# Kernel tuning notes

Measured on AMD Instinct MI355X. Metric: run time of the kernel, lower is better.

The kernel has to match this reference:

```python
import jax, jax.numpy as jnp
import numpy as np

B, S, HID, NH = 2, 2048, 2048, 16
HD = HID // NH  # 128
BASE = 10000.0


def rope_tables(seq_len, head_dim):
    inv_freq = 1.0 / (BASE ** (jnp.arange(0, head_dim, 2, dtype=jnp.float32) / head_dim))
    t = jnp.arange(seq_len, dtype=jnp.float32)
    freqs = jnp.einsum('i,j->ij', t, inv_freq)        # [s, d/2]
    emb = jnp.concatenate([freqs, freqs], axis=-1)     # [s, d]
    return jnp.cos(emb), jnp.sin(emb)


def apply_rotary(x, cos, sin):
    # x: [b, s, h, d]; cos/sin: [s, d]
    x1, x2 = x[..., ::2], x[..., 1::2]
    c = cos[None, :, None, ::2]
    s = sin[None, :, None, ::2]
    x1r = x1 * c - x2 * s
    x2r = x1 * s + x2 * c
    return jnp.stack([x1r, x2r], axis=-1).reshape(x.shape)


def setup_inputs() -> dict:
    key = jax.random.key(0)
    ks = jax.random.split(key, 5)
    scale = 1.0 / np.sqrt(HID)
    hidden_states = jax.random.normal(ks[0], (B, S, HID), jnp.float32)
    Wq = jax.random.normal(ks[1], (HID, HID), jnp.float32) * scale
    Wk = jax.random.normal(ks[2], (HID, HID), jnp.float32) * scale
    Wv = jax.random.normal(ks[3], (HID, HID), jnp.float32) * scale
    Wo = jax.random.normal(ks[4], (HID, HID), jnp.float32) * scale
    causal = jnp.tril(jnp.ones((S, S), dtype=bool))
    attention_mask = jnp.where(causal, 0.0, -1e9).astype(jnp.float32)[None, :, :]  # [1, S, S]
    return {'hidden_states': hidden_states, 'Wq': Wq, 'Wk': Wk, 'Wv': Wv,
            'Wo': Wo, 'attention_mask': attention_mask}


def reference(hidden_states, Wq, Wk, Wv, Wo, attention_mask):
    b, s, hid = hidden_states.shape
    q = (hidden_states @ Wq.T).reshape(b, s, NH, HD)
    k = (hidden_states @ Wk.T).reshape(b, s, NH, HD)
    v = (hidden_states @ Wv.T).reshape(b, s, NH, HD)
    cos, sin = rope_tables(s, HD)
    q = apply_rotary(q, cos, sin)
    k = apply_rotary(k, cos, sin)
    # [b, h, s, d]
    q = q.transpose(0, 2, 1, 3)
    k = k.transpose(0, 2, 1, 3)
    v = v.transpose(0, 2, 1, 3)
    scores = jnp.einsum('bhqd,bhkd->bhqk', q, k) / np.sqrt(HD).astype(np.float32)
    scores = scores + attention_mask[:, None, :, :]  # broadcast mask over heads
    probs = jax.nn.softmax(scores.astype(jnp.float32), axis=-1).astype(q.dtype)
    attn = jnp.einsum('bhqk,bhkd->bhqd', probs, v)
    attn = attn.transpose(0, 2, 1, 3).reshape(b, s, hid)
    return attn @ Wo.T
```

## Files before the change

kernel.cpp:

```cpp
#include <hip/hip_runtime.h>
#include <math.h>

typedef __attribute__((ext_vector_type(8))) short short8;
typedef __attribute__((ext_vector_type(4))) float f32x4;
typedef __attribute__((ext_vector_type(16))) float f32x16;
typedef __attribute__((ext_vector_type(4))) float fvec4;
typedef __attribute__((ext_vector_type(4))) unsigned short us4;
typedef __attribute__((ext_vector_type(2))) unsigned int uint2v;

#define DI __device__ __forceinline__
#define BARX asm volatile("s_barrier" ::: "memory")
#define WAITV6 asm volatile("s_waitcnt vmcnt(6)" ::: "memory")
#define WAITV0 asm volatile("s_waitcnt vmcnt(0)" ::: "memory")
#define WAITL0 asm volatile("s_waitcnt lgkmcnt(0)" ::: "memory")
#define SCHED0 __builtin_amdgcn_sched_barrier(0)

constexpr int BB = 2, SS = 2048, HIDc = 2048, NHc = 16, HDc = 128;
constexpr int MT = BB * SS;
constexpr int KC = HIDc;

constexpr size_t OFF_HB  = 0;
constexpr size_t OFF_WB  = OFF_HB + (size_t)MT * KC * 2;
constexpr size_t OFF_Q   = OFF_WB + (size_t)4 * HIDc * KC * 2;
constexpr size_t OFF_K   = OFF_Q  + (size_t)BB * NHc * SS * HDc * 2;
constexpr size_t OFF_V   = OFF_K  + (size_t)BB * NHc * SS * HDc * 2;
constexpr size_t OFF_ATT = OFF_V  + (size_t)BB * NHc * SS * HDc * 2;
constexpr size_t OFF_COS = OFF_ATT + (size_t)MT * HIDc * 2;
constexpr size_t OFF_SIN = OFF_COS + (size_t)SS * 32 * 4;
constexpr size_t WS_NEED = OFF_SIN + (size_t)SS * 32 * 4;

DI float bf2f(unsigned short u) { union { unsigned u; float f; } v; v.u = (unsigned)u << 16; return v.f; }
DI unsigned short f2bf(float f) {
  union { float f; unsigned u; } v; v.f = f;
  unsigned r = v.u + 0x7fffu + ((v.u >> 16) & 1u);
  return (unsigned short)(r >> 16);
}

DI void gload_lds16(const void* g, void* l) {
  __builtin_amdgcn_global_load_lds((const __attribute__((address_space(1))) void*)g,
                                   (__attribute__((address_space(3))) void*)l, 16, 0, 0);
}

DI unsigned cvtpk_bf16(float lo, float hi_) {
  unsigned r;
  asm("v_cvt_pk_bf16_f32 %0, %1, %2" : "=v"(r) : "v"(lo), "v"(hi_));
  return r;
}

__global__ void __launch_bounds__(256) cvt_kernel(
    const float* __restrict__ H,  const float* __restrict__ W0,
    const float* __restrict__ W1, const float* __restrict__ W2,
    const float* __restrict__ W3, unsigned short* __restrict__ dst,
    float* __restrict__ cosT, float* __restrict__ sinT)
{
  constexpr size_t HN = (size_t)MT * KC;
  constexpr size_t WN = (size_t)HIDc * KC;
  if (blockIdx.x >= 12288) {
    int idx = (blockIdx.x - 12288) * 256 + threadIdx.x;
    int t = idx >> 5, fi = idx & 31;
    float inv = powf(10000.0f, -(float)fi * (1.0f / 32.0f));
    float ang = (float)t * inv;
    cosT[idx] = cosf(ang);
    sinT[idx] = sinf(ang);
    return;
  }
  size_t e0 = ((size_t)blockIdx.x * 256 + threadIdx.x) * 8;
  const float* src; size_t off;
  if (e0 < HN) { src = H; off = e0; }
  else {
    size_t t = e0 - HN; int a = (int)(t >> 22);
    src = (a == 0) ? W0 : (a == 1) ? W1 : (a == 2) ? W2 : W3;
    off = t & (WN - 1);
  }
  fvec4 v0 = *(const fvec4*)(src + off);
  fvec4 v1 = *(const fvec4*)(src + off + 4);
  short8 o;
  o[0] = (short)f2bf(v0[0]); o[1] = (short)f2bf(v0[1]);
  o[2] = (short)f2bf(v0[2]); o[3] = (short)f2bf(v0[3]);
  o[4] = (short)f2bf(v1[0]); o[5] = (short)f2bf(v1[1]);
  o[6] = (short)f2bf(v1[2]); o[7] = (short)f2bf(v1[3]);
  *(short8*)(dst + e0) = o;
}

template<int NBX>
__global__ void __launch_bounds__(512, 2) gemm8p(
    const unsigned short* __restrict__ A,
    const unsigned short* __restrict__ Bw,
    void* __restrict__ dq, void* __restrict__ dk, void* __restrict__ dv,
    const float* __restrict__ cosT, const float* __restrict__ sinT)
{
  __shared__ __align__(16) unsigned short SL[8][128 * 64];
  const int tid = threadIdx.x, lane = tid & 63, w = tid >> 6;
  const int wm = w >> 2, wn = w & 3;
  const int ln15 = lane & 15, lq = lane >> 4;

  const int xcd = blockIdx.x & 7, idx = blockIdx.x >> 3;
  const int by = xcd * 2 + idx / NBX, bx = idx % NBX;
  const int m0 = by * 256, n0 = bx * 256;

  const int srow = tid >> 3;
  const int sc = (tid & 7) ^ (srow & 7);
  const unsigned short* Ab = A  + ((size_t)m0 + srow) * KC + sc * 8;
  const unsigned short* Bb = Bw + ((size_t)n0 + srow) * KC + sc * 8;

  constexpr int NT = KC / 64;
  auto stage = [&](int kt, bool isA, int half, int buf) {
    if (kt >= NT) return;
    const unsigned short* s = (isA ? Ab : Bb) + (size_t)(half * 128) * KC + kt * 64;
    int slot = (isA ? 0 : 4) + buf * 2 + half;
    unsigned short* d = &SL[slot][(size_t)(w * 64) * 8];
    gload_lds16(s, d);
    gload_lds16(s + (size_t)64 * KC, d + (size_t)512 * 8);
  };

  auto readA = [&](int buf, int q, int i, int ks) -> short8 {
    int rl = ((q & 1) << 6) + (i << 5) + (wm << 4) + ln15;
    return *(const short8*)&SL[buf * 2 + (q >> 1)]
        [rl * 64 + ((((ks << 2) + lq) ^ (rl & 7)) << 3)];
  };
  auto readB = [&](int buf, int j, int ks) -> short8 {
    int rl = ((wn & 1) << 6) + (j << 4) + ln15;
    return *(const short8*)&SL[4 + buf * 2 + (wn >> 1)]
        [rl * 64 + ((((ks << 2) + lq) ^ (rl & 7)) << 3)];
  };

  stage(0, true, 0, 0); stage(0, true, 1, 0);
  stage(0, false, 0, 0); stage(0, false, 1, 0);
  stage(1, false, 0, 1); stage(1, false, 1, 1); stage(1, true, 0, 1);
  WAITV6; BARX;

  f32x4 acc[8][4] = {};
  short8 bfr[4][2];
  constexpr int NIT = NT / 2;
  for (int t = 0; t < NIT; ++t) {
    const int k2 = 2 * t + 2, k3 = 2 * t + 3;
#pragma unroll
    for (int b = 0; b < 2; ++b) {
#pragma unroll
      for (int q = 0; q < 4; ++q) {
        short8 af[2][2];
#pragma unroll
        for (int i = 0; i < 2; ++i)
#pragma unroll
          for (int ks = 0; ks < 2; ++ks) af[i][ks] = readA(b, q, i, ks);
        if (q == 0) {
#pragma unroll
          for (int j = 0; j < 4; ++j)
#pragma unroll
            for (int ks = 0; ks < 2; ++ks) bfr[j][ks] = readB(b, j, ks);
        }
        if (b == 0) {
          if (q == 0) stage(2 * t + 1, true, 1, 1);
          else if (q == 1) stage(k2, false, 0, 0);
          else if (q == 2) stage(k2, false, 1, 0);
          else stage(k2, true, 0, 0);
        } else {
          if (q == 0) stage(k2, true, 1, 0);
          else if (q == 1) stage(k3, false, 0, 1);
          else if (q == 2) stage(k3, false, 1, 1);
          else stage(k3, true, 0, 1);
        }
        BARX;
        WAITL0; SCHED0;
        __builtin_amdgcn_s_setprio(1);
#pragma unroll
        for (int i = 0; i < 2; ++i)
#pragma unroll
          for (int j = 0; j < 4; ++j)
#pragma unroll
            for (int ks = 0; ks < 2; ++ks)
              acc[2 * q + i][j] = __builtin_amdgcn_mfma_f32_16x16x32_bf16(
                  af[i][ks], bfr[j][ks], acc[2 * q + i][j], 0, 0, 0);
        __builtin_amdgcn_s_setprio(0);
        if (q == 3) { if (t == NIT - 1) { WAITV0; } else { WAITV6; } }
        BARX;
      }
    }
  }

#pragma unroll
  for (int f = 0; f < 8; ++f)
#pragma unroll
    for (int j = 0; j < 4; ++j) {
      int col = n0 + wn * 64 + j * 16 + ln15;
      int z = col >> 11;
      int c2 = col & 2047;
      int h = c2 >> 7, d = c2 & 127;
      int m = m0 + 32 * f + 16 * wm + lq * 4;
      int b = m >> 11, s = m & 2047;
      if (z == 2) {
        us4 pk;
#pragma unroll
        for (int r = 0; r < 4; ++r) pk[r] = f2bf(acc[f][j][r]);
        *(us4*)((unsigned short*)dv + (((size_t)b * NHc + h) * HDc + d) * SS + s) = pk;
      } else {
        unsigned short* D = (unsigned short*)(z ? dk : dq);
        const int fi = (d >> 1) & 31;
        const bool odd = (d & 1) != 0;
#pragma unroll
        for (int r = 0; r < 4; ++r) {
          float v = acc[f][j][r];
          float p = __shfl_xor(v, 1);
          float cs = cosT[(size_t)(s + r) * 32 + fi];
          float sn = sinT[(size_t)(s + r) * 32 + fi];
          float y = odd ? (p * sn + v * cs) : (v * cs - p * sn);
          D[(((size_t)b * NHc + h) * SS + s + r) * HDc + d] = f2bf(y);
        }
      }
    }
}

template<int EPI, int NBX>
__global__ void __launch_bounds__(512, 2) gemm8(
    const unsigned short* __restrict__ A,
    const unsigned short* __restrict__ Bw,
    void* __restrict__ dq, void* __restrict__ dk, void* __restrict__ dv,
    const float* __restrict__ cosT, const float* __restrict__ sinT)
{
  __shared__ __align__(16) unsigned short Al[3][256 * 64];
  __shared__ __align__(16) unsigned short Bl[3][128 * 64];
  const int tid = threadIdx.x, lane = tid & 63, w = tid >> 6;
  const int wm = w >> 1, wn = w & 1;
  const int ln15 = lane & 15, lq = lane >> 4;

  const int xcd = blockIdx.x & 7, idx = blockIdx.x >> 3;
  const int by = xcd * 2 + idx / NBX, bx = idx % NBX;
  const int m0 = by * 256, n0 = bx * 128;

  const int srow = tid >> 3;
  const int sc = (tid & 7) ^ (srow & 7);
  const unsigned short* asrc[4];
  const unsigned short* bsrc[2];
#pragma unroll
  for (int l = 0; l < 4; ++l) asrc[l] = A  + (size_t)(m0 + l * 64 + srow) * KC + sc * 8;
#pragma unroll
  for (int l = 0; l < 2; ++l) bsrc[l] = Bw + (size_t)(n0 + l * 64 + srow) * KC + sc * 8;

  const int x7 = ln15 & 7;
  const int slA0 = (lq ^ x7) * 8;
  const int slA1 = ((4 + lq) ^ x7) * 8;
  int rA[4], rB[4];
#pragma unroll
  for (int i = 0; i < 4; ++i) rA[i] = (wm * 64 + i * 16 + ln15) * 64;
#pragma unroll
  for (int j = 0; j < 4; ++j) rB[j] = (wn * 64 + j * 16 + ln15) * 64;

  constexpr int NT = KC / 64;
  auto stA = [&](int kt, int buf, int l) {
    gload_lds16(asrc[l] + (size_t)kt * 64, &Al[buf][(size_t)(l * 512 + w * 64) * 8]);
  };
  auto stB = [&](int kt, int buf, int l) {
    gload_lds16(bsrc[l] + (size_t)kt * 64, &Bl[buf][(size_t)(l * 512 + w * 64) * 8]);
  };

  stA(0, 0, 0); stA(0, 0, 1); stA(0, 0, 2); stA(0, 0, 3); stB(0, 0, 0); stB(0, 0, 1);
  stA(1, 1, 0); stA(1, 1, 1); stA(1, 1, 2); stA(1, 1, 3); stB(1, 1, 0); stB(1, 1, 1);
  WAITV6; BARX;

  f32x4 acc[4][4] = {};
  int cb = 0, nb = 2;
  for (int kt = 0; kt < NT; ++kt) {
    const unsigned short* Ac = &Al[cb][0];
    const unsigned short* Bc = &Bl[cb][0];
    const bool pf = (kt + 2 < NT);
    short8 a01[2][2], a23[2][2], bf[4][2];

#pragma unroll
    for (int i = 0; i < 2; ++i) {
      a01[i][0] = *(const short8*)&Ac[rA[i] + slA0];
      a01[i][1] = *(const short8*)&Ac[rA[i] + slA1];
    }
#pragma unroll
    for (int j = 0; j < 4; ++j) {
      bf[j][0] = *(const short8*)&Bc[rB[j] + slA0];
      bf[j][1] = *(const short8*)&Bc[rB[j] + slA1];
    }
    if (pf) { stA(kt + 2, nb, 0); stA(kt + 2, nb, 1); stA(kt + 2, nb, 2); }
    BARX;
    WAITL0; SCHED0;
    __builtin_amdgcn_s_setprio(1);
#pragma unroll
    for (int i = 0; i < 2; ++i)
#pragma unroll
      for (int j = 0; j < 4; ++j)
#pragma unroll
        for (int k = 0; k < 2; ++k)
          acc[i][j] = __builtin_amdgcn_mfma_f32_16x16x32_bf16(a01[i][k], bf[j][k], acc[i][j], 0, 0, 0);
    __builtin_amdgcn_s_setprio(0);
    BARX;

#pragma unroll
    for (int i = 0; i < 2; ++i) {
      a23[i][0] = *(const short8*)&Ac[rA[2 + i] + slA0];
      a23[i][1] = *(const short8*)&Ac[rA[2 + i] + slA1];
    }
    if (pf) { stA(kt + 2, nb, 3); stB(kt + 2, nb, 0); stB(kt + 2, nb, 1); }
    BARX;
    WAITL0; SCHED0;
    __builtin_amdgcn_s_setprio(1);
#pragma unroll
    for (int i = 0; i < 2; ++i)
#pragma unroll
      for (int j = 0; j < 4; ++j)
#pragma unroll
        for (int k = 0; k < 2; ++k)
          acc[2 + i][j] = __builtin_amdgcn_mfma_f32_16x16x32_bf16(a23[i][k], bf[j][k], acc[2 + i][j], 0, 0, 0);
    __builtin_amdgcn_s_setprio(0);
    if (kt < NT - 2) { WAITV6; }
    else if (kt == NT - 2) { WAITV0; }
    BARX;

    cb = (cb == 2) ? 0 : cb + 1;
    nb = (nb == 2) ? 0 : nb + 1;
  }

  if (EPI == 1) {
    float* O = (float*)dq;
#pragma unroll
    for (int i = 0; i < 4; ++i)
#pragma unroll
      for (int j = 0; j < 4; ++j) {
        int col = n0 + wn * 64 + j * 16 + ln15;
        int m = m0 + wm * 64 + i * 16 + lq * 4;
#pragma unroll
        for (int r = 0; r < 4; ++r)
          O[(size_t)(m + r) * HIDc + col] = acc[i][j][r];
      }
  } else {
    unsigned short* V = (unsigned short*)dq;
#pragma unroll
    for (int i = 0; i < 4; ++i)
#pragma unroll
      for (int j = 0; j < 4; ++j) {
        int col = n0 + wn * 64 + j * 16 + ln15;
        int h = col >> 7, d = col & 127;
        int m = m0 + wm * 64 + i * 16 + lq * 4;
        int b = m >> 11, s = m & 2047;
        us4 pk;
#pragma unroll
        for (int r = 0; r < 4; ++r) pk[r] = f2bf(acc[i][j][r]);
        *(us4*)(V + (((size_t)b * NHc + h) * HDc + d) * SS + s) = pk;
      }
  }
}

__global__ void __launch_bounds__(512, 2) attn_kernel(
    const unsigned short* __restrict__ Qg,
    const unsigned short* __restrict__ Kg,
    const unsigned short* __restrict__ Vg,
    unsigned short* __restrict__ Og)
{
  __shared__ __align__(16) unsigned short Klds[2][128 * 128];
  __shared__ __align__(16) unsigned short Vlds[2][128 * 128];
  __shared__ __align__(16) unsigned short Plds[8][32 * 32];
  const int tid = threadIdx.x, lane = tid & 63, w = tid >> 6;
  const int l31 = lane & 31, hi = lane >> 5;

  const int wg = blockIdx.x;
  const int xcd = wg & 7, idx = wg >> 3;
  const int bh = xcd + 8 * (idx & 3);
  const int tt = idx >> 2;

  const int qtile = (w < 2) ? tt : (w < 4) ? (tt + 8) : (w < 6) ? (31 - tt) : (23 - tt);
  const int sub1 = w & 1;
  const int q0w = qtile * 64 + sub1 * 32;
  const int NT128 = (33 - tt) >> 1;

  const size_t hbase = (size_t)bh * SS * HDc;
  const float CE = 1.44269504089f * 0.08838834764831845f;
  const int b = bh >> 4, h = bh & 15;

  short8 qf[8];
#pragma unroll
  for (int ks = 0; ks < 8; ++ks)
    qf[ks] = *(const short8*)(Qg + hbase + (size_t)(q0w + l31) * HDc + ks * 16 + hi * 8);

  f32x16 accO[4];
#pragma unroll
  for (int db = 0; db < 4; ++db)
#pragma unroll
    for (int r = 0; r < 16; ++r) accO[db][r] = 0.f;
  float mr = -1e30f, lr = 0.f;

  auto stage = [&](int T, int buf) {
    const int kv0 = T * 128;
#pragma unroll
    for (int p = 0; p < 4; ++p) {
      int c = p * 512 + tid;
      int krow = c >> 4, ksl = c & 15;
      gload_lds16(Kg + hbase + (size_t)(kv0 + krow) * HDc + ((ksl ^ (krow & 7)) << 3),
                  (unsigned short*)&Klds[buf][0] + (size_t)c * 8);
      int vd = c >> 4, vsl = c & 15;
      gload_lds16(Vg + hbase + (size_t)vd * SS + kv0 + ((vsl ^ (vd & 7)) << 3),
                  (unsigned short*)&Vlds[buf][0] + (size_t)c * 8);
    }
  };

  stage(0, 0);
  WAITV0; BARX;

  for (int T = 0; T < NT128; ++T) {
    const int cur = T & 1;
    if (T + 1 < NT128) stage(T + 1, cur ^ 1);

#pragma unroll
    for (int sub = 0; sub < 2; ++sub) {
      const int kvt = 2 * T + sub;
      if (kvt <= qtile) {
        const bool diag = (kvt == qtile);
        const bool haveT1 = (!diag) || sub1;

        f32x16 s0, s1;
#pragma unroll
        for (int r = 0; r < 16; ++r) s0[r] = 0.f;
        __builtin_amdgcn_s_setprio(1);
#pragma unroll
        for (int ks = 0; ks < 8; ++ks) {
          int row = sub * 64 + l31;
          short8 kf = *(const short8*)&Klds[cur][row * 128 + (((2 * ks + hi) ^ (row & 7)) << 3)];
          s0 = __builtin_amdgcn_mfma_f32_32x32x16_bf16(kf, qf[ks], s0, 0, 0, 0);
        }
        if (haveT1) {
#pragma unroll
          for (int r = 0; r < 16; ++r) s1[r] = 0.f;
#pragma unroll
          for (int ks = 0; ks < 8; ++ks) {
            int row = sub * 64 + 32 + l31;
            short8 kf = *(const short8*)&Klds[cur][row * 128 + (((2 * ks + hi) ^ (row & 7)) << 3)];
            s1 = __builtin_amdgcn_mfma_f32_32x32x16_bf16(kf, qf[ks], s1, 0, 0, 0);
          }
        }
        __builtin_amdgcn_s_setprio(0);

        if (diag) {
          if (sub1) {
#pragma unroll
            for (int r = 0; r < 16; ++r)
              if (((r & 3) + 8 * (r >> 2) + 4 * hi) > l31) s1[r] = -1e30f;
          } else {
#pragma unroll
            for (int r = 0; r < 16; ++r)
              if (((r & 3) + 8 * (r >> 2) + 4 * hi) > l31) s0[r] = -1e30f;
          }
        }

        float pmax = s0[0];
#pragma unroll
        for (int r = 1; r < 16; ++r) pmax = fmaxf(pmax, s0[r]);
        if (haveT1) {
#pragma unroll
          for (int r = 0; r < 16; ++r) pmax = fmaxf(pmax, s1[r]);
        }
        pmax = fmaxf(pmax, __shfl_xor(pmax, 32));

        int grow = (CE * (pmax - mr) > 8.0f) ? 1 : 0;
        if (__any(grow)) {
          float mn = fmaxf(mr, pmax);
          float al = exp2f(CE * (mr - mn));
          mr = mn; lr *= al;
          float alr[16];
#pragma unroll
          for (int r = 0; r < 16; ++r)
            alr[r] = __shfl(al, (r & 3) + 8 * (r >> 2) + 4 * hi);
#pragma unroll
          for (int db = 0; db < 4; ++db)
#pragma unroll
            for (int r = 0; r < 16; ++r) accO[db][r] *= alr[r];
        }

        float psum = 0.f;
#pragma unroll
        for (int r = 0; r < 16; ++r) {
          float p = exp2f(CE * (s0[r] - mr));
          s0[r] = p; psum += p;
        }
        if (haveT1) {
#pragma unroll
          for (int r = 0; r < 16; ++r) {
            float p = exp2f(CE * (s1[r] - mr));
            s1[r] = p; psum += p;
          }
        }
        psum += __shfl_xor(psum, 32);
        lr += psum;

#pragma unroll
        for (int i = 0; i < 4; ++i) {
          uint2v pk;
          pk[0] = cvtpk_bf16(s0[4 * i], s0[4 * i + 1]);
          pk[1] = cvtpk_bf16(s0[4 * i + 2], s0[4 * i + 3]);
          int c = i ^ (l31 & 3);
          *(uint2v*)&Plds[w][l31 * 32 + c * 8 + hi * 4] = pk;
        }
        {
          short8 ap0 = *(const short8*)&Plds[w][l31 * 32 + ((hi ^ (l31 & 3)) << 3)];
          short8 ap1 = *(const short8*)&Plds[w][l31 * 32 + (((2 + hi) ^ (l31 & 3)) << 3)];
          __builtin_amdgcn_s_setprio(1);
#pragma unroll
          for (int db = 0; db < 4; ++db) {
            int row = db * 32 + l31;
            short8 vf0 = *(const short8*)&Vlds[cur][row * 128 + ((sub * 8 + ((0 + hi) ^ (row & 7))) << 3)];
            short8 vf1 = *(const short8*)&Vlds[cur][row * 128 + ((sub * 8 + ((2 + hi) ^ (row & 7))) << 3)];
            accO[db] = __builtin_amdgcn_mfma_f32_32x32x16_bf16(ap0, vf0, accO[db], 0, 0, 0);
            accO[db] = __builtin_amdgcn_mfma_f32_32x32x16_bf16(ap1, vf1, accO[db], 0, 0, 0);
          }
          __builtin_amdgcn_s_setprio(0);
        }

        if (haveT1) {
#pragma unroll
          for (int i = 0; i < 4; ++i) {
            uint2v pk;
            pk[0] = cvtpk_bf16(s1[4 * i], s1[4 * i + 1]);
            pk[1] = cvtpk_bf16(s1[4 * i + 2], s1[4 * i + 3]);
            int c = i ^ (l31 & 3);
            *(uint2v*)&Plds[w][l31 * 32 + c * 8 + hi * 4] = pk;
          }
          short8 ap0 = *(const short8*)&Plds[w][l31 * 32 + ((hi ^ (l31 & 3)) << 3)];
          short8 ap1 = *(const short8*)&Plds[w][l31 * 32 + (((2 + hi) ^ (l31 & 3)) << 3)];
          __builtin_amdgcn_s_setprio(1);
#pragma unroll
          for (int db = 0; db < 4; ++db) {
            int row = db * 32 + l31;
            short8 vf0 = *(const short8*)&Vlds[cur][row * 128 + ((sub * 8 + ((4 + hi) ^ (row & 7))) << 3)];
            short8 vf1 = *(const short8*)&Vlds[cur][row * 128 + ((sub * 8 + ((6 + hi) ^ (row & 7))) << 3)];
            accO[db] = __builtin_amdgcn_mfma_f32_32x32x16_bf16(ap0, vf0, accO[db], 0, 0, 0);
            accO[db] = __builtin_amdgcn_mfma_f32_32x32x16_bf16(ap1, vf1, accO[db], 0, 0, 0);
          }
          __builtin_amdgcn_s_setprio(0);
        }
      }
    }

    WAITV0; BARX;
  }

  float il = 1.0f / lr;
  float ilr[16];
#pragma unroll
  for (int r = 0; r < 16; ++r)
    ilr[r] = __shfl(il, (r & 3) + 8 * (r >> 2) + 4 * hi);
#pragma unroll
  for (int db = 0; db < 4; ++db)
#pragma unroll
    for (int r = 0; r < 16; ++r) {
      int q = q0w + (r & 3) + 8 * (r >> 2) + 4 * hi;
      int d = db * 32 + l31;
      Og[((size_t)b * SS + q) * HIDc + h * HDc + d] = f2bf(accO[db][r] * ilr[r]);
    }
}

extern "C" void kernel_launch(void* const* d_in, const int* in_sizes, int n_in,
                              void* d_out, int out_size, void* d_ws, size_t ws_size,
                              hipStream_t stream)
{
  if (ws_size < WS_NEED) return;

  const float* H  = (const float*)d_in[0];
  const float* Wq = (const float*)d_in[1];
  const float* Wk = (const float*)d_in[2];
  const float* Wv = (const float*)d_in[3];
  const float* Wo = (const float*)d_in[4];
  char* ws = (char*)d_ws;
  unsigned short* HB = (unsigned short*)(ws + OFF_HB);
  unsigned short* WB = (unsigned short*)(ws + OFF_WB);
  unsigned short* Qb = (unsigned short*)(ws + OFF_Q);
  unsigned short* Kb = (unsigned short*)(ws + OFF_K);
  unsigned short* Vb = (unsigned short*)(ws + OFF_V);
  unsigned short* AT = (unsigned short*)(ws + OFF_ATT);
  float* cosT = (float*)(ws + OFF_COS);
  float* sinT = (float*)(ws + OFF_SIN);

  cvt_kernel<<<12544, 256, 0, stream>>>(H, Wq, Wk, Wv, Wo, HB, cosT, sinT);
  gemm8p<16><<<256, 512, 0, stream>>>(HB, WB, Qb, Kb, Vb, cosT, sinT);
  gemm8<2, 16><<<256, 512, 0, stream>>>(HB, WB + (size_t)2 * HIDc * KC,
                                        Vb, nullptr, nullptr, nullptr, nullptr);
  attn_kernel<<<256, 512, 0, stream>>>(Qb, Kb, Vb, AT);
  gemm8<1, 16><<<256, 512, 0, stream>>>(AT, WB + (size_t)3 * HIDc * KC,
                                        d_out, nullptr, nullptr, nullptr, nullptr);
}
```

Baseline: 238.5 us.

## Split attention into smaller 256-thread blocks with 64-row KV tiles

The attention kernel now launches twice as many blocks of 256 threads. Each block pairs query tile t with 31-t for causal load balance, instead of four query tiles per 512-thread block. KV staging shrinks from 128-row to 64-row tiles, which cuts LDS per block so two blocks can be resident per CU. The cost is more loop iterations and barriers per block, and K/V tiles are reloaded by twice as many blocks.

```diff
diff --git a/kernel.cpp b/kernel.cpp
--- a/kernel.cpp
+++ b/kernel.cpp
@@ -344,27 +344,27 @@
   }
 }
 
-__global__ void __launch_bounds__(512, 2) attn_kernel(
+__global__ void __launch_bounds__(256, 2) attn_kernel(
     const unsigned short* __restrict__ Qg,
     const unsigned short* __restrict__ Kg,
     const unsigned short* __restrict__ Vg,
     unsigned short* __restrict__ Og)
 {
-  __shared__ __align__(16) unsigned short Klds[2][128 * 128];
-  __shared__ __align__(16) unsigned short Vlds[2][128 * 128];
-  __shared__ __align__(16) unsigned short Plds[8][32 * 32];
+  __shared__ __align__(16) unsigned short Klds[2][64 * 128];
+  __shared__ __align__(16) unsigned short Vlds[2][128 * 64];
+  __shared__ __align__(16) unsigned short Plds[4][32 * 32];
   const int tid = threadIdx.x, lane = tid & 63, w = tid >> 6;
   const int l31 = lane & 31, hi = lane >> 5;
 
   const int wg = blockIdx.x;
   const int xcd = wg & 7, idx = wg >> 3;
   const int bh = xcd + 8 * (idx & 3);
-  const int tt = idx >> 2;
-
-  const int qtile = (w < 2) ? tt : (w < 4) ? (tt + 8) : (w < 6) ? (31 - tt) : (23 - tt);
+  const int t  = idx >> 2;
+
+  const int qtile = (w < 2) ? t : (31 - t);
   const int sub1 = w & 1;
   const int q0w = qtile * 64 + sub1 * 32;
-  const int NT128 = (33 - tt) >> 1;
+  const int ntiles = 32 - t;
 
   const size_t hbase = (size_t)bh * SS * HDc;
   const float CE = 1.44269504089f * 0.08838834764831845f;
@@ -382,15 +382,15 @@
     for (int r = 0; r < 16; ++r) accO[db][r] = 0.f;
   float mr = -1e30f, lr = 0.f;
 
-  auto stage = [&](int T, int buf) {
-    const int kv0 = T * 128;
+  auto stage = [&](int kvt, int buf) {
+    const int kv0 = kvt * 64;
 #pragma unroll
     for (int p = 0; p < 4; ++p) {
-      int c = p * 512 + tid;
+      int c = p * 256 + tid;
       int krow = c >> 4, ksl = c & 15;
       gload_lds16(Kg + hbase + (size_t)(kv0 + krow) * HDc + ((ksl ^ (krow & 7)) << 3),
                   (unsigned short*)&Klds[buf][0] + (size_t)c * 8);
-      int vd = c >> 4, vsl = c & 15;
+      int vd = c >> 3, vsl = c & 7;
       gload_lds16(Vg + hbase + (size_t)vd * SS + kv0 + ((vsl ^ (vd & 7)) << 3),
                   (unsigned short*)&Vlds[buf][0] + (size_t)c * 8);
     }
@@ -399,136 +399,132 @@
   stage(0, 0);
   WAITV0; BARX;
 
-  for (int T = 0; T < NT128; ++T) {
-    const int cur = T & 1;
-    if (T + 1 < NT128) stage(T + 1, cur ^ 1);
-
-#pragma unroll
-    for (int sub = 0; sub < 2; ++sub) {
-      const int kvt = 2 * T + sub;
-      if (kvt <= qtile) {
-        const bool diag = (kvt == qtile);
-        const bool haveT1 = (!diag) || sub1;
-
-        f32x16 s0, s1;
-#pragma unroll
-        for (int r = 0; r < 16; ++r) s0[r] = 0.f;
+  for (int kvt = 0; kvt < ntiles; ++kvt) {
+    const int cur = kvt & 1;
+    if (kvt + 1 < ntiles) stage(kvt + 1, cur ^ 1);
+
+    if (kvt <= qtile) {
+      const bool diag = (kvt == qtile);
+      const bool haveT1 = (!diag) || sub1;
+
+      f32x16 s0, s1;
+#pragma unroll
+      for (int r = 0; r < 16; ++r) s0[r] = 0.f;
+      __builtin_amdgcn_s_setprio(1);
+#pragma unroll
+      for (int ks = 0; ks < 8; ++ks) {
+        int row = l31;
+        short8 kf = *(const short8*)&Klds[cur][row * 128 + (((2 * ks + hi) ^ (row & 7)) << 3)];
+        s0 = __builtin_amdgcn_mfma_f32_32x32x16_bf16(kf, qf[ks], s0, 0, 0, 0);
+      }
+      if (haveT1) {
+#pragma unroll
+        for (int r = 0; r < 16; ++r) s1[r] = 0.f;
+#pragma unroll
+        for (int ks = 0; ks < 8; ++ks) {
+          int row = 32 + l31;
+          short8 kf = *(const short8*)&Klds[cur][row * 128 + (((2 * ks + hi) ^ (row & 7)) << 3)];
+          s1 = __builtin_amdgcn_mfma_f32_32x32x16_bf16(kf, qf[ks], s1, 0, 0, 0);
+        }
+      }
+      __builtin_amdgcn_s_setprio(0);
+
+      if (diag) {
+        if (sub1) {
+#pragma unroll
+          for (int r = 0; r < 16; ++r)
+            if (((r & 3) + 8 * (r >> 2) + 4 * hi) > l31) s1[r] = -1e30f;
+        } else {
+#pragma unroll
+          for (int r = 0; r < 16; ++r)
+            if (((r & 3) + 8 * (r >> 2) + 4 * hi) > l31) s0[r] = -1e30f;
+        }
+      }
+
+      float pmax = s0[0];
+#pragma unroll
+      for (int r = 1; r < 16; ++r) pmax = fmaxf(pmax, s0[r]);
+      if (haveT1) {
+#pragma unroll
+        for (int r = 0; r < 16; ++r) pmax = fmaxf(pmax, s1[r]);
+      }
+      pmax = fmaxf(pmax, __shfl_xor(pmax, 32));
+
+      int grow = (CE * (pmax - mr) > 8.0f) ? 1 : 0;
+      if (__any(grow)) {
+        float mn = fmaxf(mr, pmax);
+        float al = exp2f(CE * (mr - mn));
+        mr = mn; lr *= al;
+        float alr[16];
+#pragma unroll
+        for (int r = 0; r < 16; ++r)
+          alr[r] = __shfl(al, (r & 3) + 8 * (r >> 2) + 4 * hi);
+#pragma unroll
+        for (int db = 0; db < 4; ++db)
+#pragma unroll
+          for (int r = 0; r < 16; ++r) accO[db][r] *= alr[r];
+      }
+
+      float psum = 0.f;
+#pragma unroll
+      for (int r = 0; r < 16; ++r) {
+        float p = exp2f(CE * (s0[r] - mr));
+        s0[r] = p; psum += p;
+      }
+      if (haveT1) {
+#pragma unroll
+        for (int r = 0; r < 16; ++r) {
+          float p = exp2f(CE * (s1[r] - mr));
+          s1[r] = p; psum += p;
+        }
+      }
+      psum += __shfl_xor(psum, 32);
+      lr += psum;
+
+#pragma unroll
+      for (int i = 0; i < 4; ++i) {
+        uint2v pk;
+        pk[0] = cvtpk_bf16(s0[4 * i], s0[4 * i + 1]);
+        pk[1] = cvtpk_bf16(s0[4 * i + 2], s0[4 * i + 3]);
+        int c = i ^ (l31 & 3);
+        *(uint2v*)&Plds[w][l31 * 32 + c * 8 + hi * 4] = pk;
+      }
+      {
+        short8 ap0 = *(const short8*)&Plds[w][l31 * 32 + ((hi ^ (l31 & 3)) << 3)];
+        short8 ap1 = *(const short8*)&Plds[w][l31 * 32 + (((2 + hi) ^ (l31 & 3)) << 3)];
         __builtin_amdgcn_s_setprio(1);
 #pragma unroll
-        for (int ks = 0; ks < 8; ++ks) {
-          int row = sub * 64 + l31;
-          short8 kf = *(const short8*)&Klds[cur][row * 128 + (((2 * ks + hi) ^ (row & 7)) << 3)];
-          s0 = __builtin_amdgcn_mfma_f32_32x32x16_bf16(kf, qf[ks], s0, 0, 0, 0);
-        }
-        if (haveT1) {
-#pragma unroll
-          for (int r = 0; r < 16; ++r) s1[r] = 0.f;
-#pragma unroll
-          for (int ks = 0; ks < 8; ++ks) {
-            int row = sub * 64 + 32 + l31;
-            short8 kf = *(const short8*)&Klds[cur][row * 128 + (((2 * ks + hi) ^ (row & 7)) << 3)];
-            s1 = __builtin_amdgcn_mfma_f32_32x32x16_bf16(kf, qf[ks], s1, 0, 0, 0);
-          }
+        for (int db = 0; db < 4; ++db) {
+          int row = db * 32 + l31;
+          short8 vf0 = *(const short8*)&Vlds[cur][row * 64 + (((0 + hi) ^ (row & 7)) << 3)];
+          short8 vf1 = *(const short8*)&Vlds[cur][row * 64 + (((2 + hi) ^ (row & 7)) << 3)];
+          accO[db] = __builtin_amdgcn_mfma_f32_32x32x16_bf16(ap0, vf0, accO[db], 0, 0, 0);
+          accO[db] = __builtin_amdgcn_mfma_f32_32x32x16_bf16(ap1, vf1, accO[db], 0, 0, 0);
         }
         __builtin_amdgcn_s_setprio(0);
-
-        if (diag) {
-          if (sub1) {
-#pragma unroll
-            for (int r = 0; r < 16; ++r)
-              if (((r & 3) + 8 * (r >> 2) + 4 * hi) > l31) s1[r] = -1e30f;
-          } else {
-#pragma unroll
-            for (int r = 0; r < 16; ++r)
-              if (((r & 3) + 8 * (r >> 2) + 4 * hi) > l31) s0[r] = -1e30f;
-          }
-        }
-
-        float pmax = s0[0];
-#pragma unroll
-        for (int r = 1; r < 16; ++r) pmax = fmaxf(pmax, s0[r]);
-        if (haveT1) {
-#pragma unroll
-          for (int r = 0; r < 16; ++r) pmax = fmaxf(pmax, s1[r]);
-        }
-        pmax = fmaxf(pmax, __shfl_xor(pmax, 32));
-
-        int grow = (CE * (pmax - mr) > 8.0f) ? 1 : 0;
-        if (__any(grow)) {
-          float mn = fmaxf(mr, pmax);
-          float al = exp2f(CE * (mr - mn));
-          mr = mn; lr *= al;
-          float alr[16];
-#pragma unroll
-          for (int r = 0; r < 16; ++r)
-            alr[r] = __shfl(al, (r & 3) + 8 * (r >> 2) + 4 * hi);
-#pragma unroll
-          for (int db = 0; db < 4; ++db)
-#pragma unroll
-            for (int r = 0; r < 16; ++r) accO[db][r] *= alr[r];
-        }
-
-        float psum = 0.f;
-#pragma unroll
-        for (int r = 0; r < 16; ++r) {
-          float p = exp2f(CE * (s0[r] - mr));
-          s0[r] = p; psum += p;
-        }
-        if (haveT1) {
-#pragma unroll
-          for (int r = 0; r < 16; ++r) {
-            float p = exp2f(CE * (s1[r] - mr));
-            s1[r] = p; psum += p;
-          }
-        }
-        psum += __shfl_xor(psum, 32);
-        lr += psum;
-
+      }
+
+      if (haveT1) {
 #pragma unroll
         for (int i = 0; i < 4; ++i) {
           uint2v pk;
-          pk[0] = cvtpk_bf16(s0[4 * i], s0[4 * i + 1]);
-          pk[1] = cvtpk_bf16(s0[4 * i + 2], s0[4 * i + 3]);
+          pk[0] = cvtpk_bf16(s1[4 * i], s1[4 * i + 1]);
+          pk[1] = cvtpk_bf16(s1[4 * i + 2], s1[4 * i + 3]);
           int c = i ^ (l31 & 3);
           *(uint2v*)&Plds[w][l31 * 32 + c * 8 + hi * 4] = pk;
         }
-        {
-          short8 ap0 = *(const short8*)&Plds[w][l31 * 32 + ((hi ^ (l31 & 3)) << 3)];
-          short8 ap1 = *(const short8*)&Plds[w][l31 * 32 + (((2 + hi) ^ (l31 & 3)) << 3)];
-          __builtin_amdgcn_s_setprio(1);
-#pragma unroll
-          for (int db = 0; db < 4; ++db) {
-            int row = db * 32 + l31;
-            short8 vf0 = *(const short8*)&Vlds[cur][row * 128 + ((sub * 8 + ((0 + hi) ^ (row & 7))) << 3)];
-            short8 vf1 = *(const short8*)&Vlds[cur][row * 128 + ((sub * 8 + ((2 + hi) ^ (row & 7))) << 3)];
-            accO[db] = __builtin_amdgcn_mfma_f32_32x32x16_bf16(ap0, vf0, accO[db], 0, 0, 0);
-            accO[db] = __builtin_amdgcn_mfma_f32_32x32x16_bf16(ap1, vf1, accO[db], 0, 0, 0);
-          }
-          __builtin_amdgcn_s_setprio(0);
-        }
-
-        if (haveT1) {
-#pragma unroll
-          for (int i = 0; i < 4; ++i) {
-            uint2v pk;
-            pk[0] = cvtpk_bf16(s1[4 * i], s1[4 * i + 1]);
-            pk[1] = cvtpk_bf16(s1[4 * i + 2], s1[4 * i + 3]);
-            int c = i ^ (l31 & 3);
-            *(uint2v*)&Plds[w][l31 * 32 + c * 8 + hi * 4] = pk;
-          }
-          short8 ap0 = *(const short8*)&Plds[w][l31 * 32 + ((hi ^ (l31 & 3)) << 3)];
-          short8 ap1 = *(const short8*)&Plds[w][l31 * 32 + (((2 + hi) ^ (l31 & 3)) << 3)];
-          __builtin_amdgcn_s_setprio(1);
-#pragma unroll
-          for (int db = 0; db < 4; ++db) {
-            int row = db * 32 + l31;
-            short8 vf0 = *(const short8*)&Vlds[cur][row * 128 + ((sub * 8 + ((4 + hi) ^ (row & 7))) << 3)];
-            short8 vf1 = *(const short8*)&Vlds[cur][row * 128 + ((sub * 8 + ((6 + hi) ^ (row & 7))) << 3)];
-            accO[db] = __builtin_amdgcn_mfma_f32_32x32x16_bf16(ap0, vf0, accO[db], 0, 0, 0);
-            accO[db] = __builtin_amdgcn_mfma_f32_32x32x16_bf16(ap1, vf1, accO[db], 0, 0, 0);
-          }
-          __builtin_amdgcn_s_setprio(0);
-        }
+        short8 ap0 = *(const short8*)&Plds[w][l31 * 32 + ((hi ^ (l31 & 3)) << 3)];
+        short8 ap1 = *(const short8*)&Plds[w][l31 * 32 + (((2 + hi) ^ (l31 & 3)) << 3)];
+        __builtin_amdgcn_s_setprio(1);
+#pragma unroll
+        for (int db = 0; db < 4; ++db) {
+          int row = db * 32 + l31;
+          short8 vf0 = *(const short8*)&Vlds[cur][row * 64 + (((4 + hi) ^ (row & 7)) << 3)];
+          short8 vf1 = *(const short8*)&Vlds[cur][row * 64 + (((6 + hi) ^ (row & 7)) << 3)];
+          accO[db] = __builtin_amdgcn_mfma_f32_32x32x16_bf16(ap0, vf0, accO[db], 0, 0, 0);
+          accO[db] = __builtin_amdgcn_mfma_f32_32x32x16_bf16(ap1, vf1, accO[db], 0, 0, 0);
+        }
+        __builtin_amdgcn_s_setprio(0);
       }
     }
 
@@ -575,7 +571,7 @@
   gemm8p<16><<<256, 512, 0, stream>>>(HB, WB, Qb, Kb, Vb, cosT, sinT);
   gemm8<2, 16><<<256, 512, 0, stream>>>(HB, WB + (size_t)2 * HIDc * KC,
                                         Vb, nullptr, nullptr, nullptr, nullptr);
-  attn_kernel<<<256, 512, 0, stream>>>(Qb, Kb, Vb, AT);
+  attn_kernel<<<512, 256, 0, stream>>>(Qb, Kb, Vb, AT);
   gemm8<1, 16><<<256, 512, 0, stream>>>(AT, WB + (size_t)3 * HIDc * KC,
                                         d_out, nullptr, nullptr, nullptr, nullptr);
 }
```

After: 240.4 us. About the same (+0.8%).
